# Performance work log

Measured on AMD Instinct MI355X. Metric: run time of the kernel, lower is better.

The kernel has to match this reference:

```python
import jax, jax.numpy as jnp
import numpy as np
import math

NUM_LEVELS = 12
FEAT = 2
LOG2_HASH = 17
HASH_SIZE = 2 ** LOG2_HASH
BASE_RES = 16
FINEST_RES = 256
N_POINTS = 1_000_000

_b = math.exp((math.log(FINEST_RES) - math.log(BASE_RES)) / (NUM_LEVELS - 1))
# static per-level grid resolutions, matching max(1, int(round(base * b**lvl)))
RESOLUTIONS = np.array([max(1, int(round(BASE_RES * _b ** l))) for l in range(NUM_LEVELS)], dtype=np.float32)
PRIMES = np.array([73856093, 19349663, 83492791], dtype=np.int32)
# the 8 trilinear corner offsets, ordered (ix, iy, iz) as in the torch loops
OFFSETS = np.array([[ix, iy, iz] for ix in (0, 1) for iy in (0, 1) for iz in (0, 1)], dtype=np.int32)


def setup_inputs() -> dict:
    key = jax.random.key(0)
    k1, k2 = jax.random.split(key)
    x = jax.random.uniform(k1, (N_POINTS, 3), dtype=jnp.float32)  # canonical coords in [0,1)
    # stacked embedding tables, init uniform(-1e-4, 1e-4) per reset_parameters
    tables = jax.random.uniform(k2, (NUM_LEVELS, HASH_SIZE, FEAT), dtype=jnp.float32,
                                minval=-1e-4, maxval=1e-4)
    return {"x": x, "tables": tables}


def reference(x, tables):
    # x: [N, 3], tables: [L, H, F] -> out: [N, L, F]
    res = jnp.asarray(RESOLUTIONS)                       # [L]
    xs = x[:, None, :] * res[None, :, None]              # [N, L, 3]
    x0f = jnp.floor(xs)
    w = xs - x0f                                         # [N, L, 3]
    x0 = x0f.astype(jnp.int32)

    offs = jnp.asarray(OFFSETS)                          # [8, 3]
    corners = x0[:, :, None, :] + offs[None, None, :, :] # [N, L, 8, 3]
    primes = jnp.asarray(PRIMES)
    # spatial hash; int32 wraparound is harmless since HASH_SIZE is a power of 2
    # dividing 2^32, so h & (HASH_SIZE-1) == torch.remainder(int64 hash, HASH_SIZE)
    h = (corners[..., 0] * primes[0]) ^ (corners[..., 1] * primes[1]) ^ (corners[..., 2] * primes[2])
    idx = h & (HASH_SIZE - 1)                            # [N, L, 8]

    lvl = jnp.arange(NUM_LEVELS)[None, :, None]          # broadcast level index
    feats = tables[lvl, idx]                             # [N, L, 8, F]

    offs_f = offs.astype(jnp.float32)                    # [8, 3]
    # trilinear weight per corner: prod over axes of (w if offset==1 else 1-w)
    wts = jnp.prod(jnp.where(offs_f[None, None, :, :] > 0,
                             w[:, :, None, :], 1.0 - w[:, :, None, :]), axis=-1)  # [N, L, 8]

    return jnp.einsum('nlc,nlcf->nlf', wts, feats)       # [N, L, F]
```

## Files before the change

kernel.cpp:

```cpp
#include <hip/hip_runtime.h>
#include <cstdint>

constexpr int kHashSize = 1 << 17;
constexpr uint32_t kHashMask = (uint32_t)kHashSize - 1u;

typedef float f2 __attribute__((ext_vector_type(2)));

__constant__ float kRes[12] = {16.f,  21.f,  26.f,  34.f,  44.f,  56.f,
                               73.f,  93.f,  120.f, 155.f, 199.f, 256.f};

__global__ __launch_bounds__(256) void hashenc_grouped(
    const float* __restrict__ x,
    const float* __restrict__ tables,
    float* __restrict__ out,
    int npts, int bpg) {
  const int b = blockIdx.x;
  const int c = b & 7;
  const int g = c >> 1;
  const int sub = ((b >> 3) << 1) | (c & 1);
  if (sub >= bpg) return;
  const int n = sub * 256 + (int)threadIdx.x;
  if (n >= npts) return;

  const float px = __builtin_nontemporal_load(x + 3 * n + 0);
  const float py = __builtin_nontemporal_load(x + 3 * n + 1);
  const float pz = __builtin_nontemporal_load(x + 3 * n + 2);

  const f2* __restrict__ tbl2 = reinterpret_cast<const f2*>(tables);

  f2 accv[3];

#pragma unroll
  for (int k = 0; k < 3; ++k) {
    const int l = 3 * g + k;
    const float r = kRes[l];
    const float xs = px * r, ys = py * r, zs = pz * r;
    const float fx = floorf(xs), fy = floorf(ys), fz = floorf(zs);
    const float wx = xs - fx, wy = ys - fy, wz = zs - fz;
    const uint32_t ix = (uint32_t)(int32_t)fx;
    const uint32_t iy = (uint32_t)(int32_t)fy;
    const uint32_t iz = (uint32_t)(int32_t)fz;

    const uint32_t hx0 = ix * 73856093u, hx1 = hx0 + 73856093u;
    const uint32_t hy0 = iy * 19349663u, hy1 = hy0 + 19349663u;
    const uint32_t hz0 = iz * 83492791u, hz1 = hz0 + 83492791u;

    const f2* __restrict__ t = tbl2 + (size_t)l * kHashSize;

    const f2 f000 = t[(hx0 ^ hy0 ^ hz0) & kHashMask];
    const f2 f001 = t[(hx0 ^ hy0 ^ hz1) & kHashMask];
    const f2 f010 = t[(hx0 ^ hy1 ^ hz0) & kHashMask];
    const f2 f011 = t[(hx0 ^ hy1 ^ hz1) & kHashMask];
    const f2 f100 = t[(hx1 ^ hy0 ^ hz0) & kHashMask];
    const f2 f101 = t[(hx1 ^ hy0 ^ hz1) & kHashMask];
    const f2 f110 = t[(hx1 ^ hy1 ^ hz0) & kHashMask];
    const f2 f111 = t[(hx1 ^ hy1 ^ hz1) & kHashMask];

    const float ax0 = 1.f - wx, ax1 = wx;
    const float by0 = 1.f - wy, by1 = wy;
    const float cz0 = 1.f - wz, cz1 = wz;
    const float ab00 = ax0 * by0, ab01 = ax0 * by1;
    const float ab10 = ax1 * by0, ab11 = ax1 * by1;
    const float w000 = ab00 * cz0, w001 = ab00 * cz1;
    const float w010 = ab01 * cz0, w011 = ab01 * cz1;
    const float w100 = ab10 * cz0, w101 = ab10 * cz1;
    const float w110 = ab11 * cz0, w111 = ab11 * cz1;

    f2 a;
    a.x = w000 * f000.x + w001 * f001.x + w010 * f010.x + w011 * f011.x +
          w100 * f100.x + w101 * f101.x + w110 * f110.x + w111 * f111.x;
    a.y = w000 * f000.y + w001 * f001.y + w010 * f010.y + w011 * f011.y +
          w100 * f100.y + w101 * f101.y + w110 * f110.y + w111 * f111.y;
    accv[k] = a;
  }

  f2* o = reinterpret_cast<f2*>(out + (size_t)n * 24 + g * 6);
  __builtin_nontemporal_store(accv[0], o + 0);
  __builtin_nontemporal_store(accv[1], o + 1);
  __builtin_nontemporal_store(accv[2], o + 2);
}

extern "C" void kernel_launch(void* const* d_in, const int* in_sizes, int n_in,
                              void* d_out, int out_size, void* d_ws, size_t ws_size,
                              hipStream_t stream) {
  const float* x = (const float*)d_in[0];
  const float* tables = (const float*)d_in[1];
  float* out = (float*)d_out;
  const int npts = in_sizes[0] / 3;
  const int bpg = (npts + 255) / 256;
  const int nblocks = 8 * ((bpg + 1) / 2);
  hipLaunchKernelGGL(hashenc_grouped, dim3(nblocks), dim3(256), 0, stream, x,
                     tables, out, npts, bpg);
}
```

Before: 488.3 us.

## Spatially bin points by counting sort before hash encoding for table locality

Adds a counting sort that bins points into a 32^3 grid (histogram with atomics, single-block scan, scatter into packed float4 with the original index), then runs the encoder on the sorted points so neighbouring threads hit nearby hash entries. It also regroups levels per block so each group mixes coarse and fine levels, balancing cache footprint. The goal is better L2 and TLB locality for the random table gathers. In exchange it adds four extra kernels, workspace traffic and scattered 8-byte output writes by original index, and it falls back to the old kernel if the workspace is too small.

```diff
diff --git a/kernel.cpp b/kernel.cpp
--- a/kernel.cpp
+++ b/kernel.cpp
@@ -3,14 +3,83 @@
 
 constexpr int kHashSize = 1 << 17;
 constexpr uint32_t kHashMask = (uint32_t)kHashSize - 1u;
+constexpr int kBuckets = 32 * 32 * 32;
 
 typedef float f2 __attribute__((ext_vector_type(2)));
+typedef float f4 __attribute__((ext_vector_type(4)));
 
 __constant__ float kRes[12] = {16.f,  21.f,  26.f,  34.f,  44.f,  56.f,
                                73.f,  93.f,  120.f, 155.f, 199.f, 256.f};
 
-__global__ __launch_bounds__(256) void hashenc_grouped(
-    const float* __restrict__ x,
+__constant__ int kGL[4][3] = {{0, 4, 11}, {1, 5, 10}, {2, 6, 9}, {3, 7, 8}};
+
+__global__ __launch_bounds__(256) void k_zero(uint32_t* hist) {
+  int i = blockIdx.x * 256 + threadIdx.x;
+  if (i < kBuckets) hist[i] = 0u;
+}
+
+__global__ __launch_bounds__(256) void k_hist(const float* __restrict__ x,
+                                              uint32_t* __restrict__ hist,
+                                              uint32_t* __restrict__ cellbuf,
+                                              uint32_t* __restrict__ rankbuf,
+                                              int npts) {
+  int n = blockIdx.x * 256 + threadIdx.x;
+  if (n >= npts) return;
+  float px = x[3 * n + 0], py = x[3 * n + 1], pz = x[3 * n + 2];
+  uint32_t ix = (uint32_t)min(31, (int)(px * 32.f));
+  uint32_t iy = (uint32_t)min(31, (int)(py * 32.f));
+  uint32_t iz = (uint32_t)min(31, (int)(pz * 32.f));
+  uint32_t cell = (ix << 10) | (iy << 5) | iz;
+  uint32_t r = atomicAdd(&hist[cell], 1u);
+  cellbuf[n] = cell;
+  rankbuf[n] = r;
+}
+
+__global__ __launch_bounds__(1024) void k_scan(uint32_t* __restrict__ hist) {
+  __shared__ uint32_t lds[1024];
+  const int t = threadIdx.x;
+  uint32_t v[32];
+  uint32_t s = 0;
+#pragma unroll
+  for (int i = 0; i < 32; ++i) {
+    v[i] = hist[t * 32 + i];
+    s += v[i];
+  }
+  lds[t] = s;
+  __syncthreads();
+  for (int off = 1; off < 1024; off <<= 1) {
+    uint32_t add = (t >= off) ? lds[t - off] : 0u;
+    __syncthreads();
+    lds[t] += add;
+    __syncthreads();
+  }
+  uint32_t run = lds[t] - s;
+#pragma unroll
+  for (int i = 0; i < 32; ++i) {
+    uint32_t c = v[i];
+    hist[t * 32 + i] = run;
+    run += c;
+  }
+}
+
+__global__ __launch_bounds__(256) void k_scatter(const float* __restrict__ x,
+                                                 const uint32_t* __restrict__ offs,
+                                                 const uint32_t* __restrict__ cellbuf,
+                                                 const uint32_t* __restrict__ rankbuf,
+                                                 f4* __restrict__ pts, int npts) {
+  int n = blockIdx.x * 256 + threadIdx.x;
+  if (n >= npts) return;
+  uint32_t pos = offs[cellbuf[n]] + rankbuf[n];
+  f4 p;
+  p.x = x[3 * n + 0];
+  p.y = x[3 * n + 1];
+  p.z = x[3 * n + 2];
+  p.w = __uint_as_float((uint32_t)n);
+  __builtin_nontemporal_store(p, pts + pos);
+}
+
+__global__ __launch_bounds__(256) void hashenc_sorted(
+    const f4* __restrict__ pts,
     const float* __restrict__ tables,
     float* __restrict__ out,
     int npts, int bpg) {
@@ -22,14 +91,72 @@
   const int n = sub * 256 + (int)threadIdx.x;
   if (n >= npts) return;
 
-  const float px = __builtin_nontemporal_load(x + 3 * n + 0);
-  const float py = __builtin_nontemporal_load(x + 3 * n + 1);
-  const float pz = __builtin_nontemporal_load(x + 3 * n + 2);
+  const f4 p = pts[n];
+  const float px = p.x, py = p.y, pz = p.z;
+  const uint32_t orig = __float_as_uint(p.w);
 
   const f2* __restrict__ tbl2 = reinterpret_cast<const f2*>(tables);
-
+  f2* __restrict__ out2 = reinterpret_cast<f2*>(out);
+
+#pragma unroll
+  for (int k = 0; k < 3; ++k) {
+    const int l = kGL[g][k];
+    const float r = kRes[l];
+    const float xs = px * r, ys = py * r, zs = pz * r;
+    const float fx = floorf(xs), fy = floorf(ys), fz = floorf(zs);
+    const float wx = xs - fx, wy = ys - fy, wz = zs - fz;
+    const uint32_t ix = (uint32_t)(int32_t)fx;
+    const uint32_t iy = (uint32_t)(int32_t)fy;
+    const uint32_t iz = (uint32_t)(int32_t)fz;
+
+    const uint32_t hx0 = ix * 73856093u, hx1 = hx0 + 73856093u;
+    const uint32_t hy0 = iy * 19349663u, hy1 = hy0 + 19349663u;
+    const uint32_t hz0 = iz * 83492791u, hz1 = hz0 + 83492791u;
+
+    const f2* __restrict__ t = tbl2 + (size_t)l * kHashSize;
+
+    const f2 f000 = t[(hx0 ^ hy0 ^ hz0) & kHashMask];
+    const f2 f001 = t[(hx0 ^ hy0 ^ hz1) & kHashMask];
+    const f2 f010 = t[(hx0 ^ hy1 ^ hz0) & kHashMask];
+    const f2 f011 = t[(hx0 ^ hy1 ^ hz1) & kHashMask];
+    const f2 f100 = t[(hx1 ^ hy0 ^ hz0) & kHashMask];
+    const f2 f101 = t[(hx1 ^ hy0 ^ hz1) & kHashMask];
+    const f2 f110 = t[(hx1 ^ hy1 ^ hz0) & kHashMask];
+    const f2 f111 = t[(hx1 ^ hy1 ^ hz1) & kHashMask];
+
+    const float ax0 = 1.f - wx, ax1 = wx;
+    const float by0 = 1.f - wy, by1 = wy;
+    const float cz0 = 1.f - wz, cz1 = wz;
+    const float ab00 = ax0 * by0, ab01 = ax0 * by1;
+    const float ab10 = ax1 * by0, ab11 = ax1 * by1;
+    const float w000 = ab00 * cz0, w001 = ab00 * cz1;
+    const float w010 = ab01 * cz0, w011 = ab01 * cz1;
+    const float w100 = ab10 * cz0, w101 = ab10 * cz1;
+    const float w110 = ab11 * cz0, w111 = ab11 * cz1;
+
+    f2 a;
+    a.x = w000 * f000.x + w001 * f001.x + w010 * f010.x + w011 * f011.x +
+          w100 * f100.x + w101 * f101.x + w110 * f110.x + w111 * f111.x;
+    a.y = w000 * f000.y + w001 * f001.y + w010 * f010.y + w011 * f011.y +
+          w100 * f100.y + w101 * f101.y + w110 * f110.y + w111 * f111.y;
+
+    __builtin_nontemporal_store(a, out2 + (size_t)orig * 12 + l);
+  }
+}
+
+__global__ __launch_bounds__(256) void hashenc_grouped(
+    const float* __restrict__ x, const float* __restrict__ tables,
+    float* __restrict__ out, int npts, int bpg) {
+  const int b = blockIdx.x;
+  const int c = b & 7;
+  const int g = c >> 1;
+  const int sub = ((b >> 3) << 1) | (c & 1);
+  if (sub >= bpg) return;
+  const int n = sub * 256 + (int)threadIdx.x;
+  if (n >= npts) return;
+  const float px = x[3 * n + 0], py = x[3 * n + 1], pz = x[3 * n + 2];
+  const f2* __restrict__ tbl2 = reinterpret_cast<const f2*>(tables);
   f2 accv[3];
-
 #pragma unroll
   for (int k = 0; k < 3; ++k) {
     const int l = 3 * g + k;
@@ -40,13 +167,10 @@
     const uint32_t ix = (uint32_t)(int32_t)fx;
     const uint32_t iy = (uint32_t)(int32_t)fy;
     const uint32_t iz = (uint32_t)(int32_t)fz;
-
     const uint32_t hx0 = ix * 73856093u, hx1 = hx0 + 73856093u;
     const uint32_t hy0 = iy * 19349663u, hy1 = hy0 + 19349663u;
     const uint32_t hz0 = iz * 83492791u, hz1 = hz0 + 83492791u;
-
     const f2* __restrict__ t = tbl2 + (size_t)l * kHashSize;
-
     const f2 f000 = t[(hx0 ^ hy0 ^ hz0) & kHashMask];
     const f2 f001 = t[(hx0 ^ hy0 ^ hz1) & kHashMask];
     const f2 f010 = t[(hx0 ^ hy1 ^ hz0) & kHashMask];
@@ -55,7 +179,6 @@
     const f2 f101 = t[(hx1 ^ hy0 ^ hz1) & kHashMask];
     const f2 f110 = t[(hx1 ^ hy1 ^ hz0) & kHashMask];
     const f2 f111 = t[(hx1 ^ hy1 ^ hz1) & kHashMask];
-
     const float ax0 = 1.f - wx, ax1 = wx;
     const float by0 = 1.f - wy, by1 = wy;
     const float cz0 = 1.f - wz, cz1 = wz;
@@ -65,7 +188,6 @@
     const float w010 = ab01 * cz0, w011 = ab01 * cz1;
     const float w100 = ab10 * cz0, w101 = ab10 * cz1;
     const float w110 = ab11 * cz0, w111 = ab11 * cz1;
-
     f2 a;
     a.x = w000 * f000.x + w001 * f001.x + w010 * f010.x + w011 * f011.x +
           w100 * f100.x + w101 * f101.x + w110 * f110.x + w111 * f111.x;
@@ -73,7 +195,6 @@
           w100 * f100.y + w101 * f101.y + w110 * f110.y + w111 * f111.y;
     accv[k] = a;
   }
-
   f2* o = reinterpret_cast<f2*>(out + (size_t)n * 24 + g * 6);
   __builtin_nontemporal_store(accv[0], o + 0);
   __builtin_nontemporal_store(accv[1], o + 1);
@@ -87,8 +208,34 @@
   const float* tables = (const float*)d_in[1];
   float* out = (float*)d_out;
   const int npts = in_sizes[0] / 3;
-  const int bpg = (npts + 255) / 256;
+  const int nb = (npts + 255) / 256;
+  const int bpg = nb;
   const int nblocks = 8 * ((bpg + 1) / 2);
-  hipLaunchKernelGGL(hashenc_grouped, dim3(nblocks), dim3(256), 0, stream, x,
-                     tables, out, npts, bpg);
-}
+
+  const size_t npad = (size_t)nb * 256;
+  const size_t off_cell = 1u << 20;
+  const size_t off_rank = off_cell + 4 * npad;
+  const size_t off_pts = off_cell + 8 * npad;
+  const size_t need = off_cell + 24 * npad;
+
+  if (ws_size >= need) {
+    uint8_t* ws = (uint8_t*)d_ws;
+    uint32_t* hist = (uint32_t*)ws;
+    uint32_t* cellbuf = (uint32_t*)(ws + off_cell);
+    uint32_t* rankbuf = (uint32_t*)(ws + off_rank);
+    f4* pts = (f4*)(ws + off_pts);
+
+    hipLaunchKernelGGL(k_zero, dim3((kBuckets + 255) / 256), dim3(256), 0,
+                       stream, hist);
+    hipLaunchKernelGGL(k_hist, dim3(nb), dim3(256), 0, stream, x, hist, cellbuf,
+                       rankbuf, npts);
+    hipLaunchKernelGGL(k_scan, dim3(1), dim3(1024), 0, stream, hist);
+    hipLaunchKernelGGL(k_scatter, dim3(nb), dim3(256), 0, stream, x, hist,
+                       cellbuf, rankbuf, pts, npts);
+    hipLaunchKernelGGL(hashenc_sorted, dim3(nblocks), dim3(256), 0, stream, pts,
+                       tables, out, npts, bpg);
+  } else {
+    hipLaunchKernelGGL(hashenc_grouped, dim3(nblocks), dim3(256), 0, stream, x,
+                       tables, out, npts, bpg);
+  }
+}
```

Result: slower. 810.6 us (+66.0%).

## Cache coarse levels in LDS dense grids and split encoding into two kernels

Applied to the files above, without the earlier changes.

Levels 0 and 1 have few enough grid vertices (17^3 and 22^3) that each block gathers their hashed entries into a dense LDS lookup table once, then interpolates from LDS instead of issuing random global gathers. A first kernel with 256 blocks of 1024 threads handles levels 0-3 for a contiguous range of points. A second kernel handles levels 4-11 in two-level chunks with vectorized 16-byte stores. This removes global gather traffic for the coarse levels but reduces parallelism for levels 2-3 to only 256 blocks and adds a second launch plus per-block LUT fill cost.

```diff
diff --git a/kernel.cpp b/kernel.cpp
--- a/kernel.cpp
+++ b/kernel.cpp
@@ -5,21 +5,143 @@
 constexpr uint32_t kHashMask = (uint32_t)kHashSize - 1u;
 
 typedef float f2 __attribute__((ext_vector_type(2)));
+typedef float f4 __attribute__((ext_vector_type(4)));
 
 __constant__ float kRes[12] = {16.f,  21.f,  26.f,  34.f,  44.f,  56.f,
                                73.f,  93.f,  120.f, 155.f, 199.f, 256.f};
 
-__global__ __launch_bounds__(256) void hashenc_grouped(
-    const float* __restrict__ x,
-    const float* __restrict__ tables,
-    float* __restrict__ out,
-    int npts, int bpg) {
+constexpr int kD0 = 17;
+constexpr int kD1 = 22;
+constexpr int kN0 = kD0 * kD0 * kD0;
+constexpr int kN1 = kD1 * kD1 * kD1;
+
+__device__ __forceinline__ f2 level_feat(int l, float px, float py, float pz,
+                                         const f2* __restrict__ tbl2) {
+  const float r = kRes[l];
+  const float xs = px * r, ys = py * r, zs = pz * r;
+  const float fx = floorf(xs), fy = floorf(ys), fz = floorf(zs);
+  const float wx = xs - fx, wy = ys - fy, wz = zs - fz;
+  const uint32_t ix = (uint32_t)(int32_t)fx;
+  const uint32_t iy = (uint32_t)(int32_t)fy;
+  const uint32_t iz = (uint32_t)(int32_t)fz;
+  const uint32_t hx0 = ix * 73856093u, hx1 = hx0 + 73856093u;
+  const uint32_t hy0 = iy * 19349663u, hy1 = hy0 + 19349663u;
+  const uint32_t hz0 = iz * 83492791u, hz1 = hz0 + 83492791u;
+  const f2* __restrict__ t = tbl2 + (size_t)l * kHashSize;
+  const f2 f000 = t[(hx0 ^ hy0 ^ hz0) & kHashMask];
+  const f2 f001 = t[(hx0 ^ hy0 ^ hz1) & kHashMask];
+  const f2 f010 = t[(hx0 ^ hy1 ^ hz0) & kHashMask];
+  const f2 f011 = t[(hx0 ^ hy1 ^ hz1) & kHashMask];
+  const f2 f100 = t[(hx1 ^ hy0 ^ hz0) & kHashMask];
+  const f2 f101 = t[(hx1 ^ hy0 ^ hz1) & kHashMask];
+  const f2 f110 = t[(hx1 ^ hy1 ^ hz0) & kHashMask];
+  const f2 f111 = t[(hx1 ^ hy1 ^ hz1) & kHashMask];
+  const float ax0 = 1.f - wx, ax1 = wx;
+  const float by0 = 1.f - wy, by1 = wy;
+  const float cz0 = 1.f - wz, cz1 = wz;
+  const float ab00 = ax0 * by0, ab01 = ax0 * by1;
+  const float ab10 = ax1 * by0, ab11 = ax1 * by1;
+  const float w000 = ab00 * cz0, w001 = ab00 * cz1;
+  const float w010 = ab01 * cz0, w011 = ab01 * cz1;
+  const float w100 = ab10 * cz0, w101 = ab10 * cz1;
+  const float w110 = ab11 * cz0, w111 = ab11 * cz1;
+  f2 a;
+  a.x = w000 * f000.x + w001 * f001.x + w010 * f010.x + w011 * f011.x +
+        w100 * f100.x + w101 * f101.x + w110 * f110.x + w111 * f111.x;
+  a.y = w000 * f000.y + w001 * f001.y + w010 * f010.y + w011 * f011.y +
+        w100 * f100.y + w101 * f101.y + w110 * f110.y + w111 * f111.y;
+  return a;
+}
+
+__device__ __forceinline__ f2 lut_feat(const f2* lut, int D, float res,
+                                       float px, float py, float pz) {
+  const float xs = px * res, ys = py * res, zs = pz * res;
+  const float fx = floorf(xs), fy = floorf(ys), fz = floorf(zs);
+  const float wx = xs - fx, wy = ys - fy, wz = zs - fz;
+  const int ix = (int)fx, iy = (int)fy, iz = (int)fz;
+  const int i000 = (ix * D + iy) * D + iz;
+  const f2 f000 = lut[i000],            f001 = lut[i000 + 1];
+  const f2 f010 = lut[i000 + D],        f011 = lut[i000 + D + 1];
+  const f2 f100 = lut[i000 + D * D],    f101 = lut[i000 + D * D + 1];
+  const f2 f110 = lut[i000 + D * D + D], f111 = lut[i000 + D * D + D + 1];
+  const float ax0 = 1.f - wx, ax1 = wx;
+  const float by0 = 1.f - wy, by1 = wy;
+  const float cz0 = 1.f - wz, cz1 = wz;
+  const float ab00 = ax0 * by0, ab01 = ax0 * by1;
+  const float ab10 = ax1 * by0, ab11 = ax1 * by1;
+  const float w000 = ab00 * cz0, w001 = ab00 * cz1;
+  const float w010 = ab01 * cz0, w011 = ab01 * cz1;
+  const float w100 = ab10 * cz0, w101 = ab10 * cz1;
+  const float w110 = ab11 * cz0, w111 = ab11 * cz1;
+  f2 a;
+  a.x = w000 * f000.x + w001 * f001.x + w010 * f010.x + w011 * f011.x +
+        w100 * f100.x + w101 * f101.x + w110 * f110.x + w111 * f111.x;
+  a.y = w000 * f000.y + w001 * f001.y + w010 * f010.y + w011 * f011.y +
+        w100 * f100.y + w101 * f101.y + w110 * f110.y + w111 * f111.y;
+  return a;
+}
+
+__global__ __launch_bounds__(1024) void henc_A(const float* __restrict__ x,
+                                               const float* __restrict__ tables,
+                                               float* __restrict__ out,
+                                               int npts, int ppb) {
+  __shared__ f2 lut[kN0 + kN1];
+  const int t = threadIdx.x;
+  const f2* __restrict__ tbl2 = reinterpret_cast<const f2*>(tables);
+
+  for (int i = t; i < kN0; i += 1024) {
+    int iz = i % kD0;
+    int rr = i / kD0;
+    int iy = rr % kD0;
+    int ix = rr / kD0;
+    uint32_t h = (uint32_t)ix * 73856093u ^ (uint32_t)iy * 19349663u ^
+                 (uint32_t)iz * 83492791u;
+    lut[i] = tbl2[h & kHashMask];
+  }
+  for (int i = t; i < kN1; i += 1024) {
+    int iz = i % kD1;
+    int rr = i / kD1;
+    int iy = rr % kD1;
+    int ix = rr / kD1;
+    uint32_t h = (uint32_t)ix * 73856093u ^ (uint32_t)iy * 19349663u ^
+                 (uint32_t)iz * 83492791u;
+    lut[kN0 + i] = tbl2[(size_t)kHashSize + (h & kHashMask)];
+  }
+  __syncthreads();
+
+  const int base = blockIdx.x * ppb;
+  for (int i = t; i < ppb; i += 1024) {
+    const int n = base + i;
+    if (n >= npts) continue;
+    const float px = __builtin_nontemporal_load(x + 3 * n + 0);
+    const float py = __builtin_nontemporal_load(x + 3 * n + 1);
+    const float pz = __builtin_nontemporal_load(x + 3 * n + 2);
+
+    const f2 a0 = lut_feat(lut, kD0, 16.f, px, py, pz);
+    const f2 a1 = lut_feat(lut + kN0, kD1, 21.f, px, py, pz);
+    const f2 a2 = level_feat(2, px, py, pz, tbl2);
+    const f2 a3 = level_feat(3, px, py, pz, tbl2);
+
+    f4 v0, v1;
+    v0.x = a0.x; v0.y = a0.y; v0.z = a1.x; v0.w = a1.y;
+    v1.x = a2.x; v1.y = a2.y; v1.z = a3.x; v1.w = a3.y;
+    f4* o = reinterpret_cast<f4*>(out + (size_t)n * 24);
+    __builtin_nontemporal_store(v0, o + 0);
+    __builtin_nontemporal_store(v1, o + 1);
+  }
+}
+
+__global__ __launch_bounds__(256) void henc_B(const float* __restrict__ x,
+                                              const float* __restrict__ tables,
+                                              float* __restrict__ out,
+                                              int npts, int nb2) {
   const int b = blockIdx.x;
   const int c = b & 7;
-  const int g = c >> 1;
-  const int sub = ((b >> 3) << 1) | (c & 1);
-  if (sub >= bpg) return;
-  const int n = sub * 256 + (int)threadIdx.x;
+  const int r = b >> 3;
+  const int chunk = c >> 1;
+  const int half = c & 1;
+  const int pblk = half * nb2 + r;
+  const int n = pblk * 256 + (int)threadIdx.x;
   if (n >= npts) return;
 
   const float px = __builtin_nontemporal_load(x + 3 * n + 0);
@@ -27,57 +149,14 @@
   const float pz = __builtin_nontemporal_load(x + 3 * n + 2);
 
   const f2* __restrict__ tbl2 = reinterpret_cast<const f2*>(tables);
+  const int l0 = 4 + 2 * chunk;
+  const f2 a = level_feat(l0, px, py, pz, tbl2);
+  const f2 b2 = level_feat(l0 + 1, px, py, pz, tbl2);
 
-  f2 accv[3];
-
-#pragma unroll
-  for (int k = 0; k < 3; ++k) {
-    const int l = 3 * g + k;
-    const float r = kRes[l];
-    const float xs = px * r, ys = py * r, zs = pz * r;
-    const float fx = floorf(xs), fy = floorf(ys), fz = floorf(zs);
-    const float wx = xs - fx, wy = ys - fy, wz = zs - fz;
-    const uint32_t ix = (uint32_t)(int32_t)fx;
-    const uint32_t iy = (uint32_t)(int32_t)fy;
-    const uint32_t iz = (uint32_t)(int32_t)fz;
-
-    const uint32_t hx0 = ix * 73856093u, hx1 = hx0 + 73856093u;
-    const uint32_t hy0 = iy * 19349663u, hy1 = hy0 + 19349663u;
-    const uint32_t hz0 = iz * 83492791u, hz1 = hz0 + 83492791u;
-
-    const f2* __restrict__ t = tbl2 + (size_t)l * kHashSize;
-
-    const f2 f000 = t[(hx0 ^ hy0 ^ hz0) & kHashMask];
-    const f2 f001 = t[(hx0 ^ hy0 ^ hz1) & kHashMask];
-    const f2 f010 = t[(hx0 ^ hy1 ^ hz0) & kHashMask];
-    const f2 f011 = t[(hx0 ^ hy1 ^ hz1) & kHashMask];
-    const f2 f100 = t[(hx1 ^ hy0 ^ hz0) & kHashMask];
-    const f2 f101 = t[(hx1 ^ hy0 ^ hz1) & kHashMask];
-    const f2 f110 = t[(hx1 ^ hy1 ^ hz0) & kHashMask];
-    const f2 f111 = t[(hx1 ^ hy1 ^ hz1) & kHashMask];
-
-    const float ax0 = 1.f - wx, ax1 = wx;
-    const float by0 = 1.f - wy, by1 = wy;
-    const float cz0 = 1.f - wz, cz1 = wz;
-    const float ab00 = ax0 * by0, ab01 = ax0 * by1;
-    const float ab10 = ax1 * by0, ab11 = ax1 * by1;
-    const float w000 = ab00 * cz0, w001 = ab00 * cz1;
-    const float w010 = ab01 * cz0, w011 = ab01 * cz1;
-    const float w100 = ab10 * cz0, w101 = ab10 * cz1;
-    const float w110 = ab11 * cz0, w111 = ab11 * cz1;
-
-    f2 a;
-    a.x = w000 * f000.x + w001 * f001.x + w010 * f010.x + w011 * f011.x +
-          w100 * f100.x + w101 * f101.x + w110 * f110.x + w111 * f111.x;
-    a.y = w000 * f000.y + w001 * f001.y + w010 * f010.y + w011 * f011.y +
-          w100 * f100.y + w101 * f101.y + w110 * f110.y + w111 * f111.y;
-    accv[k] = a;
-  }
-
-  f2* o = reinterpret_cast<f2*>(out + (size_t)n * 24 + g * 6);
-  __builtin_nontemporal_store(accv[0], o + 0);
-  __builtin_nontemporal_store(accv[1], o + 1);
-  __builtin_nontemporal_store(accv[2], o + 2);
+  f4 v;
+  v.x = a.x; v.y = a.y; v.z = b2.x; v.w = b2.y;
+  __builtin_nontemporal_store(
+      v, reinterpret_cast<f4*>(out + (size_t)n * 24 + 8 + 4 * chunk));
 }
 
 extern "C" void kernel_launch(void* const* d_in, const int* in_sizes, int n_in,
@@ -87,8 +166,12 @@
   const float* tables = (const float*)d_in[1];
   float* out = (float*)d_out;
   const int npts = in_sizes[0] / 3;
-  const int bpg = (npts + 255) / 256;
-  const int nblocks = 8 * ((bpg + 1) / 2);
-  hipLaunchKernelGGL(hashenc_grouped, dim3(nblocks), dim3(256), 0, stream, x,
-                     tables, out, npts, bpg);
+  const int nb = (npts + 255) / 256;
+  const int nb2 = (nb + 1) / 2;
+  const int ppb = (npts + 255) / 256;
+
+  hipLaunchKernelGGL(henc_A, dim3(256), dim3(1024), 0, stream, x, tables, out,
+                     npts, ppb);
+  hipLaunchKernelGGL(henc_B, dim3(8 * nb2), dim3(256), 0, stream, x, tables,
+                     out, npts, nb2);
 }
```

After: 458.3 us. 6.1% less time.
